# Performance work log

Measured on AMD Instinct MI355X. Metric: run time of the kernel, lower is better.

## Reference

```python
import jax, jax.numpy as jnp
import numpy as np

STATE_DIM = 1024
INPUT_DIM = 1024
OUTPUT_DIM = 1024
BATCH = 8
SEQ = 2048


def setup_inputs() -> dict:
    key = jax.random.key(0)
    k_x, k_a, k_b, k_w, k_bias = jax.random.split(key, 5)
    x = jax.random.normal(k_x, (BATCH, SEQ, INPUT_DIM), dtype=jnp.float32)
    # diagonal transition a in (0, 0.99) for stability
    A = jax.random.uniform(k_a, (STATE_DIM,), dtype=jnp.float32, minval=0.0, maxval=0.99)
    B = jax.random.normal(k_b, (STATE_DIM, INPUT_DIM), dtype=jnp.float32) / np.sqrt(INPUT_DIM)
    W = jax.random.normal(k_w, (OUTPUT_DIM, STATE_DIM), dtype=jnp.float32) / np.sqrt(STATE_DIM)
    b = jax.random.normal(k_bias, (OUTPUT_DIM,), dtype=jnp.float32) * 0.01
    return {"x": x, "A": A, "B": B, "W": W, "b": b}


def reference(x, A, B, W, b):
    # x: [batch, seq, input_dim]
    # Input projection: u_t = B x_t  -> [batch, seq, state_dim]
    u = jnp.einsum('bld,nd->bln', x, B)
    # Diagonal linear recurrence h_t = A * h_{t-1} + u_t via associative scan.
    # Pair representation (a, b) composes as (a1*a2, a2*b1 + b2).
    aa = jnp.broadcast_to(A, u.shape)

    def combine(c1, c2):
        a1, b1 = c1
        a2, b2 = c2
        return a1 * a2, a2 * b1 + b2

    _, h = jax.lax.associative_scan(combine, (aa, u), axis=1)
    # Output projection: [batch, seq, output_dim]
    return jnp.einsum('bln,on->blo', h, W) + b
```

## Files before the change

kernel.cpp:

```cpp
#include <hip/hip_runtime.h>
#include <stdint.h>

#define BATCH 8
#define SEQ 2048
#define DIM 1024
#define MTOT (BATCH * SEQ)

typedef __attribute__((ext_vector_type(8))) short short8;
typedef __attribute__((ext_vector_type(8))) unsigned short ushort8;
typedef __attribute__((ext_vector_type(4))) float floatx4;


__device__ __forceinline__ unsigned short f2bf(float f) {
  union { float f; unsigned u; } c; c.f = f;
  unsigned u = c.u;
  return (unsigned short)((u + 0x7FFFu + ((u >> 16) & 1u)) >> 16);
}
__device__ __forceinline__ float bf2f(unsigned short h) {
  union { unsigned u; float f; } c; c.u = ((unsigned)h) << 16;
  return c.f;
}

__device__ __forceinline__ void gll16(const void* g, void* l) {
  __builtin_amdgcn_global_load_lds(
      (__attribute__((address_space(1))) void*)(uintptr_t)g,
      (__attribute__((address_space(3))) void*)(uintptr_t)l,
      16, 0, 0);
}


#define X4 (MTOT * DIM / 4)
#define M4 (DIM * DIM / 4)

__global__ __launch_bounds__(256) void cast3_kernel(
    const float* __restrict__ x, const float* __restrict__ B,
    const float* __restrict__ W, unsigned short* __restrict__ xb,
    unsigned short* __restrict__ Bb, unsigned short* __restrict__ Wb) {
  int i = blockIdx.x * 256 + threadIdx.x;
  const float4* s4;
  uint2* d2;
  int li;
  if (i < X4) {
    s4 = (const float4*)x; d2 = (uint2*)xb; li = i;
  } else if (i < X4 + M4) {
    s4 = (const float4*)B; d2 = (uint2*)Bb; li = i - X4;
  } else {
    s4 = (const float4*)W; d2 = (uint2*)Wb; li = i - X4 - M4;
  }
  float4 v = s4[li];
  uint2 o;
  o.x = (unsigned)f2bf(v.x) | ((unsigned)f2bf(v.y) << 16);
  o.y = (unsigned)f2bf(v.z) | ((unsigned)f2bf(v.w) << 16);
  d2[li] = o;
}


__global__ __launch_bounds__(256) void gemm1_fused(
    const unsigned short* __restrict__ A,
    const unsigned short* __restrict__ B,
    unsigned short* __restrict__ u,
    const float* __restrict__ Adiag,
    float* __restrict__ aggbuf) {
  __shared__ unsigned short smem[16384];
  __shared__ float segsum[2][128];
  unsigned short* sA = smem;
  unsigned short* sB = smem + 8192;

  const int tid = threadIdx.x;
  const int wave = tid >> 6, lane = tid & 63;

  const int id = blockIdx.x;
  const int xcd = id & 7, j = id >> 3;
  const int mt = xcd * 16 + (j >> 3);
  const int nt = j & 7;
  const size_t m0 = (size_t)mt * 128;
  const int n0 = nt * 128;

  floatx4 acc[4][4] = {};

  const int srow = wave * 8 + (lane >> 3);
  const int scol = (((lane & 7) ^ ((lane >> 3) & 7)) * 8);
  const unsigned short* gA = A + (m0 + srow) * 1024 + scol;
  const unsigned short* gB = B + ((size_t)n0 + srow) * 1024 + scol;
  unsigned short* lA = sA + wave * 8 * 64;
  unsigned short* lB = sB + wave * 8 * 64;

  const int fr = lane & 15;
  const int frs = fr & 7;
  const int kb = lane >> 4;
  const int wm = (wave & 1) * 64, wn = (wave >> 1) * 64;

  for (int kt = 0; kt < 1024; kt += 64) {
#pragma unroll
    for (int r = 0; r < 4; ++r) {
      gll16(gA + (size_t)r * 32 * 1024 + kt, lA + r * 32 * 64);
      gll16(gB + (size_t)r * 32 * 1024 + kt, lB + r * 32 * 64);
    }
    asm volatile("s_waitcnt vmcnt(0)" ::: "memory");
    __syncthreads();
#pragma unroll
    for (int kk = 0; kk < 64; kk += 32) {
      short8 af[4], bfv[4];
#pragma unroll
      for (int i = 0; i < 4; ++i)
        af[i] = *(const short8*)(sA + (wm + i * 16 + fr) * 64 +
                                 ((((kk >> 3) + kb) ^ frs) * 8));
#pragma unroll
      for (int jj = 0; jj < 4; ++jj)
        bfv[jj] = *(const short8*)(sB + (wn + jj * 16 + fr) * 64 +
                                   ((((kk >> 3) + kb) ^ frs) * 8));
#pragma unroll
      for (int i = 0; i < 4; ++i)
#pragma unroll
        for (int jj = 0; jj < 4; ++jj)
          acc[i][jj] = __builtin_amdgcn_mfma_f32_16x16x32_bf16(
              af[i], bfv[jj], acc[i][jj], 0, 0, 0);
    }
    __syncthreads();
  }

  const int col = lane & 15;
  const int row4 = (lane >> 4) * 4;
  unsigned short* sC = smem;
#pragma unroll
  for (int i = 0; i < 4; ++i)
#pragma unroll
    for (int jj = 0; jj < 4; ++jj)
#pragma unroll
      for (int r = 0; r < 4; ++r)
        sC[(wm + i * 16 + row4 + r) * 128 + wn + jj * 16 + col] =
            f2bf(acc[i][jj][r]);
  __syncthreads();

  const int colv = tid & 127;
  const int seg = tid >> 7;
  const float a = Adiag[n0 + colv];
  {
    float s = 0.f;
    const int t0 = seg * 64;
#pragma unroll 8
    for (int t = 0; t < 64; ++t) {
      int idx = (t0 + t) * 128 + colv;
      s = fmaf(a, s, bf2f(sC[idx]));
      sC[idx] = f2bf(s);
    }
    segsum[seg][colv] = s;
  }
  __syncthreads();

  {
    float a2 = a * a, a4 = a2 * a2, a8 = a4 * a4, a16 = a8 * a8;
    float a32 = a16 * a16, a64 = a32 * a32;
    const float s0 = segsum[0][colv];
    const int t0 = 64 + seg * 32;
    float apow = seg ? a32 * a : a;
#pragma unroll 8
    for (int t = 0; t < 32; ++t) {
      int idx = (t0 + t) * 128 + colv;
      sC[idx] = f2bf(fmaf(apow, s0, bf2f(sC[idx])));
      apow *= a;
    }
    if (seg)
      aggbuf[(size_t)mt * 1024 + n0 + colv] =
          fmaf(a64, s0, segsum[1][colv]);
  }
  __syncthreads();

#pragma unroll
  for (int s = 0; s < 8; ++s) {
    int row = wave * 32 + s * 4 + (lane >> 4);
    int c8 = (lane & 15) * 8;
    *(ushort8*)(u + (m0 + row) * (size_t)1024 + n0 + c8) =
        *(const ushort8*)(sC + row * 128 + c8);
  }
}


__global__ __launch_bounds__(256) void combine_kernel(
    const float* __restrict__ agg, float* __restrict__ carry,
    const float* __restrict__ Adiag) {
  const int id = blockIdx.x * 256 + threadIdx.x;
  const int b = id >> 10, n = id & (DIM - 1);
  float a = Adiag[n];
  float aL = a;
#pragma unroll
  for (int i = 0; i < 7; ++i) aL *= aL;
  float s = 0.f;
#pragma unroll
  for (int c = 0; c < 16; ++c) {
    size_t idx = (size_t)(b * 16 + c) * 1024 + n;
    float local = agg[idx];
    carry[idx] = s;
    s = fmaf(aL, s, local);
  }
}


__global__ __launch_bounds__(256) void apply_kernel(
    unsigned short* __restrict__ u, const float* __restrict__ Adiag,
    const float* __restrict__ carry) {
  const int id = blockIdx.x;
  const int xcd = id & 7, rem = id >> 3;
  const int mt = xcd * 16 + (rem >> 4);
  const int sub = rem & 15;
  const int tg = threadIdx.x >> 7;
  const int ch0 = (threadIdx.x & 127) * 8;

  float a[8], cf[8];
  *(float4*)&a[0] = *(const float4*)(Adiag + ch0);
  *(float4*)&a[4] = *(const float4*)(Adiag + ch0 + 4);
  const float* cp = carry + (size_t)mt * 1024 + ch0;
  *(float4*)&cf[0] = *(const float4*)cp;
  *(float4*)&cf[4] = *(const float4*)(cp + 4);

  const int tl = sub * 8 + tg * 4;
  float apow[8];
#pragma unroll
  for (int j = 0; j < 8; ++j)
    apow[j] = __builtin_amdgcn_exp2f(__builtin_amdgcn_logf(a[j]) *
                                     (float)(tl + 1));
  const size_t base = ((size_t)mt * 128 + tl) * DIM + ch0;
#pragma unroll
  for (int s = 0; s < 4; ++s) {
    ushort8 v = *(const ushort8*)(u + base + (size_t)s * DIM);
    ushort8 o;
#pragma unroll
    for (int j = 0; j < 8; ++j) {
      o[j] = f2bf(fmaf(apow[j], cf[j], bf2f(v[j])));
      apow[j] *= a[j];
    }
    *(ushort8*)(u + base + (size_t)s * DIM) = o;
  }
}


__global__ __launch_bounds__(512, 2) void gemm2_pipe(
    const unsigned short* __restrict__ A,
    const unsigned short* __restrict__ Bw,
    float* __restrict__ C, const float* __restrict__ bias) {
  extern __shared__ unsigned short sm[];

  const int tid = threadIdx.x;
  const int wid = tid >> 6, lane = tid & 63;

  const int id = blockIdx.x;
  const int xcd = id & 7, j = id >> 3;
  const int mt = xcd * 8 + (j >> 3);
  const int nt = j & 7;
  const size_t m0 = (size_t)mt * 256;
  const int n0 = nt * 128;

  floatx4 acc[4][4] = {};

  const int srow = tid >> 3;
  const int scolg = (tid & 7) ^ (srow & 7);
  const unsigned short* gA = A + (m0 + srow) * 1024 + scolg * 8;
  const unsigned short* gB = Bw + ((size_t)n0 + srow) * 1024 + scolg * 8;

  const int fr = lane & 15;
  const int frs = fr & 7;
  const int kb = lane >> 4;
  const int wm = (wid >> 1) * 64;
  const int wn = (wid & 1) * 64;

#define G2_STAGE(tt, s)                                                     \
  {                                                                         \
    const int kt_ = (tt) * 64;                                              \
    unsigned short* a_ = sm + (s) * 16384 + wid * 512;                      \
    unsigned short* b_ = sm + 49152 + (s) * 8192 + wid * 512;               \
    _Pragma("unroll") for (int r = 0; r < 4; ++r)                           \
        gll16(gA + (size_t)r * 64 * 1024 + kt_, a_ + r * 4096);             \
    _Pragma("unroll") for (int r = 0; r < 2; ++r)                           \
        gll16(gB + (size_t)r * 64 * 1024 + kt_, b_ + r * 4096);             \
  }

  G2_STAGE(0, 0);
  G2_STAGE(1, 1);
  asm volatile("s_waitcnt vmcnt(6)" ::: "memory");
  __syncthreads();

  for (int t = 0; t < 16; ++t) {
    if (t + 2 < 16) G2_STAGE(t + 2, (t + 2) % 3);

    const unsigned short* sA = sm + (t % 3) * 16384;
    const unsigned short* sB = sm + 49152 + (t % 3) * 8192;
    short8 af[4][2], bfv[4][2];
#pragma unroll
    for (int kk = 0; kk < 2; ++kk) {
#pragma unroll
      for (int i = 0; i < 4; ++i)
        af[i][kk] = *(const short8*)(sA + (wm + i * 16 + fr) * 64 +
                                     (((kk * 4 + kb) ^ frs) * 8));
#pragma unroll
      for (int jj = 0; jj < 4; ++jj)
        bfv[jj][kk] = *(const short8*)(sB + (wn + jj * 16 + fr) * 64 +
                                       (((kk * 4 + kb) ^ frs) * 8));
    }
    __builtin_amdgcn_s_setprio(1);
#pragma unroll
    for (int kk = 0; kk < 2; ++kk)
#pragma unroll
      for (int i = 0; i < 4; ++i)
#pragma unroll
        for (int jj = 0; jj < 4; ++jj)
          acc[i][jj] = __builtin_amdgcn_mfma_f32_16x16x32_bf16(
              af[i][kk], bfv[jj][kk], acc[i][jj], 0, 0, 0);
    __builtin_amdgcn_s_setprio(0);

    if (t + 2 < 16)
      asm volatile("s_waitcnt vmcnt(6)" ::: "memory");
    else
      asm volatile("s_waitcnt vmcnt(0)" ::: "memory");
    __syncthreads();
  }
#undef G2_STAGE

  const int col = lane & 15;
  const int row4 = (lane >> 4) * 4;
#pragma unroll
  for (int i = 0; i < 4; ++i)
#pragma unroll
    for (int jj = 0; jj < 4; ++jj)
#pragma unroll
      for (int r = 0; r < 4; ++r) {
        size_t m = m0 + wm + i * 16 + row4 + r;
        int n = n0 + wn + jj * 16 + col;
        C[m * 1024 + n] = acc[i][jj][r] + bias[n];
      }
}


extern "C" void kernel_launch(void* const* d_in, const int* in_sizes, int n_in,
                              void* d_out, int out_size, void* d_ws,
                              size_t ws_size, hipStream_t stream) {
  const float* x    = (const float*)d_in[0];
  const float* A    = (const float*)d_in[1];
  const float* B    = (const float*)d_in[2];
  const float* W    = (const float*)d_in[3];
  const float* bias = (const float*)d_in[4];

  char* ws = (char*)d_ws;
  unsigned short* xb   = (unsigned short*)ws;
  unsigned short* ubuf = (unsigned short*)(ws + 33554432);
  unsigned short* Bb   = (unsigned short*)(ws + 67108864);
  unsigned short* Wb   = (unsigned short*)(ws + 69206016);
  float* aggbuf        = (float*)(ws + 71303168);
  float* carry         = (float*)(ws + 71827456);

  static bool attr_set = false;
  if (!attr_set) {
    hipFuncSetAttribute(reinterpret_cast<const void*>(gemm2_pipe),
                        hipFuncAttributeMaxDynamicSharedMemorySize, 147456);
    attr_set = true;
  }

  cast3_kernel<<<(X4 + 2 * M4) / 256, 256, 0, stream>>>(x, B, W, xb, Bb, Wb);

  gemm1_fused<<<1024, 256, 0, stream>>>(xb, Bb, ubuf, A, aggbuf);

  combine_kernel<<<32, 256, 0, stream>>>(aggbuf, carry, A);

  apply_kernel<<<2048, 256, 0, stream>>>(ubuf, A, carry);

  gemm2_pipe<<<512, 512, 147456, stream>>>(ubuf, Wb, (float*)d_out, bias);
}
```

Before: 229.6 us.

## Pipeline gemm1 with triple-buffered LDS and larger 256x128 tiles

Replaces the single-buffered 128x128 input-projection GEMM with a 512-thread, 256x128-tile kernel. It uses a 3-stage global_load_lds pipeline with partial vmcnt waits and raises wave priority around the MFMA block. The goal is to overlap global-to-LDS transfers with matrix math and improve B-operand reuse. The fused in-block scan now handles two 128-row chunks per block, and aggbuf keeps its per-128-row layout. In exchange it needs 144KB of dynamic LDS, which limits occupancy to one block per CU.

```diff
diff --git a/kernel.cpp b/kernel.cpp
--- a/kernel.cpp
+++ b/kernel.cpp
@@ -55,73 +55,94 @@
 }
 
 
-__global__ __launch_bounds__(256) void gemm1_fused(
+__global__ __launch_bounds__(512, 2) void gemm1_pipe(
     const unsigned short* __restrict__ A,
     const unsigned short* __restrict__ B,
     unsigned short* __restrict__ u,
     const float* __restrict__ Adiag,
     float* __restrict__ aggbuf) {
-  __shared__ unsigned short smem[16384];
-  __shared__ float segsum[2][128];
-  unsigned short* sA = smem;
-  unsigned short* sB = smem + 8192;
+  extern __shared__ unsigned short sm[];
 
   const int tid = threadIdx.x;
-  const int wave = tid >> 6, lane = tid & 63;
+  const int wid = tid >> 6, lane = tid & 63;
 
   const int id = blockIdx.x;
   const int xcd = id & 7, j = id >> 3;
-  const int mt = xcd * 16 + (j >> 3);
+  const int mt2 = xcd * 8 + (j >> 3);
   const int nt = j & 7;
-  const size_t m0 = (size_t)mt * 128;
+  const size_t m0 = (size_t)mt2 * 256;
   const int n0 = nt * 128;
 
   floatx4 acc[4][4] = {};
 
-  const int srow = wave * 8 + (lane >> 3);
-  const int scol = (((lane & 7) ^ ((lane >> 3) & 7)) * 8);
-  const unsigned short* gA = A + (m0 + srow) * 1024 + scol;
-  const unsigned short* gB = B + ((size_t)n0 + srow) * 1024 + scol;
-  unsigned short* lA = sA + wave * 8 * 64;
-  unsigned short* lB = sB + wave * 8 * 64;
+  const int srow = tid >> 3;
+  const int scolg = (tid & 7) ^ (srow & 7);
+  const unsigned short* gA = A + (m0 + srow) * 1024 + scolg * 8;
+  const unsigned short* gB = B + ((size_t)n0 + srow) * 1024 + scolg * 8;
 
   const int fr = lane & 15;
   const int frs = fr & 7;
   const int kb = lane >> 4;
-  const int wm = (wave & 1) * 64, wn = (wave >> 1) * 64;
-
-  for (int kt = 0; kt < 1024; kt += 64) {
-#pragma unroll
-    for (int r = 0; r < 4; ++r) {
-      gll16(gA + (size_t)r * 32 * 1024 + kt, lA + r * 32 * 64);
-      gll16(gB + (size_t)r * 32 * 1024 + kt, lB + r * 32 * 64);
-    }
-    asm volatile("s_waitcnt vmcnt(0)" ::: "memory");
-    __syncthreads();
-#pragma unroll
-    for (int kk = 0; kk < 64; kk += 32) {
-      short8 af[4], bfv[4];
+  const int wm = (wid >> 1) * 64;
+  const int wn = (wid & 1) * 64;
+
+#define G1_STAGE(tt, s)                                                     \
+  {                                                                         \
+    const int kt_ = (tt) * 64;                                              \
+    unsigned short* a_ = sm + (s) * 16384 + wid * 512;                      \
+    unsigned short* b_ = sm + 49152 + (s) * 8192 + wid * 512;               \
+    _Pragma("unroll") for (int r = 0; r < 4; ++r)                           \
+        gll16(gA + (size_t)r * 64 * 1024 + kt_, a_ + r * 4096);             \
+    _Pragma("unroll") for (int r = 0; r < 2; ++r)                           \
+        gll16(gB + (size_t)r * 64 * 1024 + kt_, b_ + r * 4096);             \
+  }
+
+  G1_STAGE(0, 0);
+  G1_STAGE(1, 1);
+  asm volatile("s_waitcnt vmcnt(6)" ::: "memory");
+  __syncthreads();
+
+  for (int t = 0; t < 16; ++t) {
+    if (t + 2 < 16) G1_STAGE(t + 2, (t + 2) % 3);
+
+    const unsigned short* sA = sm + (t % 3) * 16384;
+    const unsigned short* sB = sm + 49152 + (t % 3) * 8192;
+    short8 af[4][2], bfv[4][2];
+#pragma unroll
+    for (int kk = 0; kk < 2; ++kk) {
 #pragma unroll
       for (int i = 0; i < 4; ++i)
-        af[i] = *(const short8*)(sA + (wm + i * 16 + fr) * 64 +
-                                 ((((kk >> 3) + kb) ^ frs) * 8));
+        af[i][kk] = *(const short8*)(sA + (wm + i * 16 + fr) * 64 +
+                                     (((kk * 4 + kb) ^ frs) * 8));
 #pragma unroll
       for (int jj = 0; jj < 4; ++jj)
-        bfv[jj] = *(const short8*)(sB + (wn + jj * 16 + fr) * 64 +
-                                   ((((kk >> 3) + kb) ^ frs) * 8));
+        bfv[jj][kk] = *(const short8*)(sB + (wn + jj * 16 + fr) * 64 +
+                                       (((kk * 4 + kb) ^ frs) * 8));
+    }
+    __builtin_amdgcn_s_setprio(1);
+#pragma unroll
+    for (int kk = 0; kk < 2; ++kk)
 #pragma unroll
       for (int i = 0; i < 4; ++i)
 #pragma unroll
         for (int jj = 0; jj < 4; ++jj)
           acc[i][jj] = __builtin_amdgcn_mfma_f32_16x16x32_bf16(
-              af[i], bfv[jj], acc[i][jj], 0, 0, 0);
-    }
+              af[i][kk], bfv[jj][kk], acc[i][jj], 0, 0, 0);
+    __builtin_amdgcn_s_setprio(0);
+
+    if (t + 2 < 16)
+      asm volatile("s_waitcnt vmcnt(6)" ::: "memory");
+    else
+      asm volatile("s_waitcnt vmcnt(0)" ::: "memory");
     __syncthreads();
   }
+#undef G1_STAGE
+
+  unsigned short* sC = sm;
+  float* segsum = (float*)(sm + 32768);
 
   const int col = lane & 15;
   const int row4 = (lane >> 4) * 4;
-  unsigned short* sC = smem;
 #pragma unroll
   for (int i = 0; i < 4; ++i)
 #pragma unroll
@@ -132,44 +153,45 @@
             f2bf(acc[i][jj][r]);
   __syncthreads();
 
+  const int ch = tid >> 8;
+  const int seg = (tid >> 7) & 1;
   const int colv = tid & 127;
-  const int seg = tid >> 7;
   const float a = Adiag[n0 + colv];
   {
     float s = 0.f;
-    const int t0 = seg * 64;
+    const int rbase = ch * 128 + seg * 64;
 #pragma unroll 8
     for (int t = 0; t < 64; ++t) {
-      int idx = (t0 + t) * 128 + colv;
+      int idx = (rbase + t) * 128 + colv;
       s = fmaf(a, s, bf2f(sC[idx]));
       sC[idx] = f2bf(s);
     }
-    segsum[seg][colv] = s;
+    segsum[(ch * 2 + seg) * 128 + colv] = s;
   }
   __syncthreads();
 
   {
     float a2 = a * a, a4 = a2 * a2, a8 = a4 * a4, a16 = a8 * a8;
     float a32 = a16 * a16, a64 = a32 * a32;
-    const float s0 = segsum[0][colv];
+    const float s0 = segsum[(ch * 2) * 128 + colv];
     const int t0 = 64 + seg * 32;
     float apow = seg ? a32 * a : a;
 #pragma unroll 8
     for (int t = 0; t < 32; ++t) {
-      int idx = (t0 + t) * 128 + colv;
+      int idx = (ch * 128 + t0 + t) * 128 + colv;
       sC[idx] = f2bf(fmaf(apow, s0, bf2f(sC[idx])));
       apow *= a;
     }
     if (seg)
-      aggbuf[(size_t)mt * 1024 + n0 + colv] =
-          fmaf(a64, s0, segsum[1][colv]);
+      aggbuf[(size_t)(mt2 * 2 + ch) * 1024 + n0 + colv] =
+          fmaf(a64, s0, segsum[(ch * 2 + 1) * 128 + colv]);
   }
   __syncthreads();
 
 #pragma unroll
   for (int s = 0; s < 8; ++s) {
-    int row = wave * 32 + s * 4 + (lane >> 4);
-    int c8 = (lane & 15) * 8;
+    int row = s * 32 + (tid >> 4);
+    int c8 = (tid & 15) * 8;
     *(ushort8*)(u + (m0 + row) * (size_t)1024 + n0 + c8) =
         *(const ushort8*)(sC + row * 128 + c8);
   }
@@ -349,6 +371,8 @@
 
   static bool attr_set = false;
   if (!attr_set) {
+    hipFuncSetAttribute(reinterpret_cast<const void*>(gemm1_pipe),
+                        hipFuncAttributeMaxDynamicSharedMemorySize, 147456);
     hipFuncSetAttribute(reinterpret_cast<const void*>(gemm2_pipe),
                         hipFuncAttributeMaxDynamicSharedMemorySize, 147456);
     attr_set = true;
@@ -356,7 +380,7 @@
 
   cast3_kernel<<<(X4 + 2 * M4) / 256, 256, 0, stream>>>(x, B, W, xb, Bb, Wb);
 
-  gemm1_fused<<<1024, 256, 0, stream>>>(xb, Bb, ubuf, A, aggbuf);
+  gemm1_pipe<<<512, 512, 147456, stream>>>(xb, Bb, ubuf, A, aggbuf);
 
   combine_kernel<<<32, 256, 0, stream>>>(aggbuf, carry, A);
 
```

After: 223.7 us. 2.6% less time.
